# Performance work log

Hardware: AMD Instinct MI355X
Metric: run time of the kernel (lower is better)

## Reference

```python
import jax, jax.numpy as jnp
import numpy as np

B = 1000        # graphs in batch
T_PER = 250     # tasks per graph
M_PER = 50      # machines per graph
N_T = B * T_PER
N_M = B * M_PER
D_T = 16        # INPUT_TASK_DIM
D_M = 8         # INPUT_MACHINE_DIM
H = 128         # hidden_dim
IN_PREV_IDX = 0
TASK_FEAT_IDX = 1
EPS = 1e-5      # BatchNorm eps


def _mk_params(rng):
    def lin(i, o):
        return (rng.standard_normal((i, o)).astype(np.float32) / np.sqrt(i),
                np.zeros(o, np.float32))
    p = {}
    p['bn_t_gamma'] = np.ones(D_T, np.float32); p['bn_t_beta'] = np.zeros(D_T, np.float32)
    p['Wt1'], p['bt1'] = lin(D_T, H); p['Wt2'], p['bt2'] = lin(H, H)
    p['bn_m_gamma'] = np.ones(D_M, np.float32); p['bn_m_beta'] = np.zeros(D_M, np.float32)
    p['Wm1'], p['bm1'] = lin(D_M, H); p['Wm2'], p['bm2'] = lin(H, H)
    p['Wa1'], p['ba1'] = lin(2 * H, H); p['Wa2'], p['ba2'] = lin(H, H)
    p['Wl1'], p['bl1'] = lin(3 * H, H); p['Wl2'], p['bl2'] = lin(H, H)
    p['Wo1'], p['bo1'] = lin(H, H); p['Wo2'], p['bo2'] = lin(H, 1)
    return p


def setup_inputs() -> dict:
    rng = np.random.default_rng(0)
    xt = rng.standard_normal((N_T, D_T)).astype(np.float32)
    # prev-task flag: even task ids are 'prev'
    xt[:, IN_PREV_IDX] = (np.arange(N_T) % 2 == 0).astype(np.float32)
    # per-graph machine assignment in [0, M_PER), or -1 (unassigned) every 10th task
    lm = rng.integers(0, M_PER, N_T)
    lm[np.arange(N_T) % 10 == 0] = -1
    xt[:, TASK_FEAT_IDX] = lm.astype(np.float32)
    xm = rng.standard_normal((N_M, D_M)).astype(np.float32)
    inp = {'x_tasks': jnp.asarray(xt), 'x_machines': jnp.asarray(xm)}
    inp.update({k: jnp.asarray(v) for k, v in _mk_params(rng).items()})
    inp['x_tasks_batch'] = jnp.asarray(np.repeat(np.arange(B), T_PER).astype(np.int32))
    inp['x_machines_batch'] = jnp.asarray(np.repeat(np.arange(B), M_PER).astype(np.int32))
    # labels are tasks 0,5,10,...; prev tasks are even ids -> prev-local index t//2
    # label tasks that are prev: t % 10 == 0 -> prev_tasks_label_idx = 5*arange(N_T//10)
    inp['label_idx'] = jnp.asarray((5 * np.arange(N_T // 10)).astype(np.int32))
    inp['num_graphs'] = B
    return inp


def _bn(x, g, b):
    # BatchNorm1d in training mode: biased batch stats
    mu = x.mean(axis=0)
    var = x.var(axis=0)
    return g * (x - mu) * jax.lax.rsqrt(var + EPS) + b


def _seg_mean(x, seg, n):
    s = jax.ops.segment_sum(x, seg, num_segments=n)
    c = jax.ops.segment_sum(jnp.ones((x.shape[0], 1), x.dtype), seg, num_segments=n)
    return s / jnp.maximum(c, 1.0)


def reference(x_tasks, x_machines, bn_t_gamma, bn_t_beta, Wt1, bt1, Wt2, bt2,
              bn_m_gamma, bn_m_beta, Wm1, bm1, Wm2, bm2,
              Wa1, ba1, Wa2, ba2, Wl1, bl1, Wl2, bl2,
              Wo1, bo1, Wo2, bo2,
              x_tasks_batch, x_machines_batch, label_idx, num_graphs):
    nm = x_machines.shape[0]
    # tasks_select_assignment: local machine id -> global machine row (or pad row nm)
    tm_col = x_tasks[:, TASK_FEAT_IDX]
    cnt_m = jnp.bincount(x_machines_batch, length=num_graphs)
    cum = jnp.cumsum(cnt_m) - cnt_m  # cumulative machines per graph
    task_m = jnp.where(tm_col == -1.0, nm,
                       tm_col.astype(jnp.int32) + cum[x_tasks_batch].astype(jnp.int32))
    # node embeddings: BN -> Linear -> ReLU -> Linear -> ReLU
    th = jax.nn.relu(jax.nn.relu(_bn(x_tasks, bn_t_gamma, bn_t_beta) @ Wt1 + bt1) @ Wt2 + bt2)
    mh = jax.nn.relu(jax.nn.relu(_bn(x_machines, bn_m_gamma, bn_m_beta) @ Wm1 + bm1) @ Wm2 + bm2)
    # global aggregation per graph (scatter_mean) + MLP
    aggr = jnp.concatenate([_seg_mean(th, x_tasks_batch, num_graphs),
                            _seg_mean(mh, x_machines_batch, num_graphs)], axis=1)
    aggr = jax.nn.relu(aggr @ Wa1 + ba1) @ Wa2 + ba2
    # gather machine embedding per task (pad row of zeros for unassigned)
    mh_pad = jnp.concatenate([mh, jnp.zeros((1, H), mh.dtype)], axis=0)
    cat = jnp.concatenate([th, aggr[x_tasks_batch], mh_pad[task_m]], axis=1)  # [N_T, 3H]
    h = jax.nn.relu(cat @ Wl1 + bl1) @ Wl2 + bl2
    out = (jax.nn.relu(h @ Wo1 + bo1) @ Wo2 + bo2)[label_idx]
    return out
```

## Files before the change

kernel.cpp:

```cpp
#include <hip/hip_runtime.h>
#include <hip/hip_bf16.h>

constexpr int B     = 1000;
constexpr int T_PER = 250;
constexpr int M_PER = 50;
constexpr int N_T   = B * T_PER;
constexpr int N_M   = B * M_PER;
constexpr int H     = 128;
constexpr int N_LBL = 25000;
constexpr float EPS = 1e-05f;

constexpr int NB_T = 256;
constexpr int NB_M = 64;
constexpr int NB_P = 64;

constexpr int OFF_PART_T = 0;
constexpr int OFF_PART_M = OFF_PART_T + NB_T * 32;
constexpr int OFF_AT     = OFF_PART_M + NB_M * 16;
constexpr int OFF_BT     = OFF_AT + 16;
constexpr int OFF_AM     = OFF_BT + 16;
constexpr int OFF_BM     = OFF_AM + 8;
constexpr int OFF_BT1F   = OFF_BM + 8;
constexpr int OFF_BM1F   = OFF_BT1F + 128;
constexpr int OFF_MEANT  = OFF_BM1F + 128;
constexpr int OFF_MEANM  = OFF_MEANT + B * H;
constexpr int OFF_HALF   = OFF_MEANM + B * H;
constexpr int HO_WT1  = 0;
constexpr int HO_WT2  = 4096;
constexpr int HO_WM1  = 20480;
constexpr int HO_WM2  = 24576;
constexpr int HO_WA1  = 40960;
constexpr int HO_WA2  = 73728;
constexpr int HO_WL1  = 90112;
constexpr int HO_WL2  = 139264;
constexpr int HO_WO1  = 155648;

typedef _Float16 f16x8 __attribute__((ext_vector_type(8)));
typedef _Float16 f16x4 __attribute__((ext_vector_type(4)));
typedef float f32x4 __attribute__((ext_vector_type(4)));

#define MFMA16(a, b, c) __builtin_amdgcn_mfma_f32_16x16x32_f16(a, b, c, 0, 0, 0)

template <int C, int NB>
__device__ __forceinline__ void stats_body(const float* __restrict__ x, int nelem,
                                           float* __restrict__ part, int blk, int t,
                                           float* ls, float* lq) {
    float s = 0.f, q = 0.f;
    for (int e = blk * 256 + t; e < nelem; e += NB * 256) {
        float v = x[e];
        s += v;
        q += v * v;
    }
    ls[t] = s; lq[t] = q;
    __syncthreads();
    if (t < C) {
        float S = 0.f, Q = 0.f;
        for (int u = t; u < 256; u += C) { S += ls[u]; Q += lq[u]; }
        part[blk * 2 * C + t] = S;
        part[blk * 2 * C + C + t] = Q;
    }
}

__device__ __forceinline__ void cvt_tr(const float* __restrict__ src, _Float16* __restrict__ dst,
                                       int K, int Kp, int tid, int nt) {
    for (int idx = tid; idx < 128 * Kp; idx += nt) {
        int c = idx / Kp, k = idx - c * Kp;
        float v = (k < K) ? src[k * 128 + c] : 0.f;
        dst[idx] = (_Float16)v;
    }
}

__global__ __launch_bounds__(256) void stats_prep_kernel(
        const float* __restrict__ xt, const float* __restrict__ xm,
        const float* __restrict__ Wt1, const float* __restrict__ Wt2,
        const float* __restrict__ Wm1, const float* __restrict__ Wm2,
        const float* __restrict__ Wa1, const float* __restrict__ Wa2,
        const float* __restrict__ Wl1, const float* __restrict__ Wl2,
        const float* __restrict__ Wo1,
        float* __restrict__ wsf, _Float16* __restrict__ wh) {
    __shared__ float ls[256], lq[256];
    const int bid = blockIdx.x, t = threadIdx.x;
    if (bid < NB_T) {
        stats_body<16, NB_T>(xt, N_T * 16, wsf + OFF_PART_T, bid, t, ls, lq);
    } else if (bid < NB_T + NB_M) {
        stats_body<8, NB_M>(xm, N_M * 8, wsf + OFF_PART_M, bid - NB_T, t, ls, lq);
    } else {
        const int tid = (bid - NB_T - NB_M) * 256 + t;
        const int nt = NB_P * 256;
        cvt_tr(Wt1, wh + HO_WT1, 16, 32, tid, nt);
        cvt_tr(Wt2, wh + HO_WT2, 128, 128, tid, nt);
        cvt_tr(Wm1, wh + HO_WM1, 8, 32, tid, nt);
        cvt_tr(Wm2, wh + HO_WM2, 128, 128, tid, nt);
        cvt_tr(Wa1, wh + HO_WA1, 256, 256, tid, nt);
        cvt_tr(Wa2, wh + HO_WA2, 128, 128, tid, nt);
        cvt_tr(Wl1, wh + HO_WL1, 384, 384, tid, nt);
        cvt_tr(Wl2, wh + HO_WL2, 128, 128, tid, nt);
        cvt_tr(Wo1, wh + HO_WO1, 128, 128, tid, nt);
    }
}

__global__ __launch_bounds__(256) void finalize_kernel(
        const float* __restrict__ gt, const float* __restrict__ btb,
        const float* __restrict__ gm, const float* __restrict__ bmb,
        const float* __restrict__ Wt1, const float* __restrict__ bt1,
        const float* __restrict__ Wm1, const float* __restrict__ bm1,
        float* __restrict__ ws) {
    __shared__ float red[256];
    __shared__ float statT[32], statM[16];
    __shared__ float shT[16], shM[8];
    const int t = threadIdx.x;
    {
        const int slot = t & 31, chunk = t >> 5;
        const float* p = ws + OFF_PART_T;
        float s = 0.f;
        for (int b = chunk * 32; b < chunk * 32 + 32; b++) s += p[b * 32 + slot];
        red[t] = s;
    }
    __syncthreads();
    if (t < 32) {
        float v = 0.f;
#pragma unroll
        for (int c = 0; c < 8; c++) v += red[t + 32 * c];
        statT[t] = v;
    }
    __syncthreads();
    {
        float s = 0.f;
        if (t < 128) {
            const int slot = t & 15, chunk = t >> 4;
            const float* p = ws + OFF_PART_M;
            for (int b = chunk * 8; b < chunk * 8 + 8; b++) s += p[b * 16 + slot];
        }
        red[t] = s;
    }
    __syncthreads();
    if (t < 16) {
        float v = 0.f;
#pragma unroll
        for (int c = 0; c < 8; c++) v += red[t + 16 * c];
        statM[t] = v;
    }
    __syncthreads();
    if (t < 16) {
        float mu  = statT[t] / (float)N_T;
        float var = statT[16 + t] / (float)N_T - mu * mu;
        float a   = gt[t] * rsqrtf(var + EPS);
        ws[OFF_AT + t] = a;
        float b = btb[t] - mu * a;
        ws[OFF_BT + t] = b;
        shT[t] = b;
    } else if (t < 24) {
        int c = t - 16;
        float mu  = statM[c] / (float)N_M;
        float var = statM[8 + c] / (float)N_M - mu * mu;
        float a   = gm[c] * rsqrtf(var + EPS);
        ws[OFF_AM + c] = a;
        float b = bmb[c] - mu * a;
        ws[OFF_BM + c] = b;
        shM[c] = b;
    }
    __syncthreads();
    if (t < 128) {
        float s = bt1[t];
#pragma unroll
        for (int k = 0; k < 16; k++) s += shT[k] * Wt1[k * 128 + t];
        ws[OFF_BT1F + t] = s;
    } else {
        int c = t - 128;
        float s = bm1[c];
#pragma unroll
        for (int k = 0; k < 8; k++) s += shM[k] * Wm1[k * 128 + c];
        ws[OFF_BM1F + c] = s;
    }
}

__device__ __forceinline__ void zacc(f32x4 acc[4][2]) {
#pragma unroll
    for (int rg = 0; rg < 4; rg++)
#pragma unroll
        for (int mi = 0; mi < 2; mi++) acc[rg][mi] = (f32x4){0.f, 0.f, 0.f, 0.f};
}

__device__ __forceinline__ void ld32(f16x8 w[2], const _Float16* __restrict__ WT,
                                     int m0, int r, int gq) {
#pragma unroll
    for (int mi = 0; mi < 2; mi++)
        w[mi] = *(const f16x8*)(WT + ((m0 + mi) * 16 + r) * 32 + gq * 8);
}

__device__ __forceinline__ void ld128(f16x8 w[2][4], const _Float16* __restrict__ WT,
                                      int lda, int k0, int m0, int r, int gq) {
#pragma unroll
    for (int mi = 0; mi < 2; mi++)
#pragma unroll
        for (int ks = 0; ks < 4; ks++)
            w[mi][ks] = *(const f16x8*)(WT + ((m0 + mi) * 16 + r) * lda + k0 + ks * 32 + gq * 8);
}

__device__ __forceinline__ void mm32(const f16x8 w[2], const _Float16* __restrict__ act,
                                     int rstride, int r, int gq, f32x4 acc[4][2]) {
#pragma unroll
    for (int rg = 0; rg < 4; rg++) {
        const f16x8 bf = *(const f16x8*)(act + (rg * 16 + r) * rstride + gq * 8);
        acc[rg][0] = MFMA16(w[0], bf, acc[rg][0]);
        acc[rg][1] = MFMA16(w[1], bf, acc[rg][1]);
    }
}

__device__ __forceinline__ void mm128(const f16x8 w[2][4], const _Float16* __restrict__ act,
                                      int rstride, int r, int gq, f32x4 acc[4][2]) {
#pragma unroll
    for (int rg = 0; rg < 4; rg++)
#pragma unroll
        for (int ks = 0; ks < 4; ks++) {
            const f16x8 bf = *(const f16x8*)(act + (rg * 16 + r) * rstride + ks * 32 + gq * 8);
            acc[rg][0] = MFMA16(w[0][ks], bf, acc[rg][0]);
            acc[rg][1] = MFMA16(w[1][ks], bf, acc[rg][1]);
        }
}

__device__ __forceinline__ void epi_cs(const f32x4 acc[4][2], const f32x4 bv[2],
                                       _Float16* __restrict__ dst, int dstride,
                                       int m0, int r, int gq, bool relu) {
#pragma unroll
    for (int rg = 0; rg < 4; rg++)
#pragma unroll
        for (int mi = 0; mi < 2; mi++) {
            f16x4 hv;
#pragma unroll
            for (int j = 0; j < 4; j++) {
                float v = acc[rg][mi][j] + bv[mi][j];
                if (relu) v = fmaxf(v, 0.f);
                hv[j] = (_Float16)v;
            }
            *(f16x4*)(dst + (rg * 16 + r) * dstride + (m0 + mi) * 16 + gq * 4) = hv;
        }
}

template <int CIN, int ROWS, int PASSES>
__device__ __forceinline__ void seg_body(const float* __restrict__ x, const float* __restrict__ scaleA,
        const _Float16* __restrict__ W1T, const float* __restrict__ b1,
        const _Float16* __restrict__ W2T, const float* __restrict__ b2,
        float* __restrict__ meanout, int g, int t,
        _Float16* __restrict__ xs, _Float16* __restrict__ h1s) {
    const int lane = t & 63, wave = t >> 6;
    const int r = lane & 15, gq = lane >> 4;
    const int m0 = 2 * wave;
    f16x8 w1[2], w2[2][4];
    ld32(w1, W1T, m0, r, gq);
    ld128(w2, W2T, 128, 0, m0, r, gq);
    f32x4 b1v[2], b2v[2];
#pragma unroll
    for (int mi = 0; mi < 2; mi++) {
        b1v[mi] = *(const f32x4*)(b1 + (m0 + mi) * 16 + gq * 4);
        b2v[mi] = *(const f32x4*)(b2 + (m0 + mi) * 16 + gq * 4);
    }
    const int jrow = (CIN == 16) ? (t >> 2) : (t >> 1);
    const int part = (CIN == 16) ? (t & 3) : (t & 1);
    const bool stager = (CIN == 16) ? true : (t < 128);
    f32x4 av = {0.f, 0.f, 0.f, 0.f};
    if (stager) av = *(const f32x4*)(scaleA + part * 4);
    f16x4 z4; z4[0] = z4[1] = z4[2] = z4[3] = (_Float16)0.f;
    if (stager) {
        if (CIN == 16) {
            *(f16x4*)(xs + jrow * 40 + 16 + part * 4) = z4;
        } else {
#pragma unroll
            for (int q = 0; q < 3; q++)
                *(f16x4*)(xs + jrow * 40 + 8 + part * 12 + q * 4) = z4;
        }
    }
    float4 xr = {0.f, 0.f, 0.f, 0.f};
    if (stager) {
        int cl = (jrow < ROWS) ? jrow : (ROWS - 1);
        xr = *(const float4*)(x + (g * ROWS + cl) * CIN + part * 4);
    }
    f32x4 rs[2];
    rs[0] = (f32x4){0.f, 0.f, 0.f, 0.f};
    rs[1] = (f32x4){0.f, 0.f, 0.f, 0.f};
    for (int p = 0; p < PASSES; p++) {
        if (stager) {
            const bool valid = (p * 64 + jrow) < ROWS;
            f16x4 hv;
            hv[0] = (_Float16)(valid ? av[0] * xr.x : 0.f);
            hv[1] = (_Float16)(valid ? av[1] * xr.y : 0.f);
            hv[2] = (_Float16)(valid ? av[2] * xr.z : 0.f);
            hv[3] = (_Float16)(valid ? av[3] * xr.w : 0.f);
            *(f16x4*)(xs + jrow * 40 + part * 4) = hv;
        }
        __syncthreads();
        if (p + 1 < PASSES && stager) {
            int lr = (p + 1) * 64 + jrow;
            int cl = (lr < ROWS) ? lr : (ROWS - 1);
            xr = *(const float4*)(x + (g * ROWS + cl) * CIN + part * 4);
        }
        f32x4 acc[4][2];
        zacc(acc);
        mm32(w1, xs, 40, r, gq, acc);
        epi_cs(acc, b1v, h1s, 136, m0, r, gq, true);
        __syncthreads();
        zacc(acc);
        mm128(w2, h1s, 136, r, gq, acc);
#pragma unroll
        for (int rg = 0; rg < 4; rg++) {
            const bool vr = (p * 64 + rg * 16 + r) < ROWS;
#pragma unroll
            for (int mi = 0; mi < 2; mi++)
#pragma unroll
                for (int j = 0; j < 4; j++) {
                    float v = fmaxf(acc[rg][mi][j] + b2v[mi][j], 0.f);
                    rs[mi][j] += vr ? v : 0.f;
                }
        }
    }
#pragma unroll
    for (int mi = 0; mi < 2; mi++)
#pragma unroll
        for (int j = 0; j < 4; j++) {
            float v = rs[mi][j];
            v += __shfl_xor(v, 1); v += __shfl_xor(v, 2);
            v += __shfl_xor(v, 4); v += __shfl_xor(v, 8);
            rs[mi][j] = v;
        }
    if (r == 0) {
        constexpr float inv = 1.f / (float)ROWS;
#pragma unroll
        for (int mi = 0; mi < 2; mi++) {
            f32x4 st = rs[mi] * inv;
            *(f32x4*)(meanout + g * H + (m0 + mi) * 16 + gq * 4) = st;
        }
    }
}

__global__ __launch_bounds__(256) void seg_fused(const float* __restrict__ xt, const float* __restrict__ xm,
        const _Float16* __restrict__ wh, const float* __restrict__ wsf,
        const float* __restrict__ bt2, const float* __restrict__ bm2,
        float* __restrict__ meanT, float* __restrict__ meanM) {
    __shared__ __attribute__((aligned(16))) _Float16 xs[64 * 40];
    __shared__ __attribute__((aligned(16))) _Float16 h1s[64 * 136];
    if (blockIdx.x < B)
        seg_body<16, T_PER, 4>(xt, wsf + OFF_AT, wh + HO_WT1, wsf + OFF_BT1F,
                               wh + HO_WT2, bt2, meanT, blockIdx.x, threadIdx.x, xs, h1s);
    else
        seg_body<8, M_PER, 1>(xm, wsf + OFF_AM, wh + HO_WM1, wsf + OFF_BM1F,
                              wh + HO_WM2, bm2, meanM, blockIdx.x - B, threadIdx.x, xs, h1s);
}

__global__ __launch_bounds__(256) void aggr_kernel(const float* __restrict__ meanT, const float* __restrict__ meanM,
        const _Float16* __restrict__ Wa1T, const float* __restrict__ ba1,
        const _Float16* __restrict__ Wa2T, const float* __restrict__ ba2,
        const _Float16* __restrict__ Wl1T, const float* __restrict__ bl1,
        float* __restrict__ agg2) {
    __shared__ __attribute__((aligned(16))) _Float16 cin[16 * 264];
    __shared__ __attribute__((aligned(16))) _Float16 h1s[16 * 136];
    __shared__ __attribute__((aligned(16))) _Float16 ags[16 * 136];
    const int t = threadIdx.x, lane = t & 63, wave = t >> 6;
    const int r = lane & 15, gq = lane >> 4;
    const int m0 = 2 * wave;
    const int g0 = blockIdx.x * 16;
    f16x8 wa1[2][8], wa2[2][4], wl1b[2][4];
#pragma unroll
    for (int mi = 0; mi < 2; mi++)
#pragma unroll
        for (int ks = 0; ks < 8; ks++)
            wa1[mi][ks] = *(const f16x8*)(Wa1T + ((m0 + mi) * 16 + r) * 256 + ks * 32 + gq * 8);
    ld128(wa2, Wa2T, 128, 0, m0, r, gq);
    ld128(wl1b, Wl1T, 384, 128, m0, r, gq);
    f32x4 b1v[2], b2v[2], blv[2];
#pragma unroll
    for (int mi = 0; mi < 2; mi++) {
        b1v[mi] = *(const f32x4*)(ba1 + (m0 + mi) * 16 + gq * 4);
        b2v[mi] = *(const f32x4*)(ba2 + (m0 + mi) * 16 + gq * 4);
        blv[mi] = *(const f32x4*)(bl1 + (m0 + mi) * 16 + gq * 4);
    }
    for (int e = t; e < 16 * 64; e += 256) {
        int j = e >> 6, c4 = e & 63;
        int g = g0 + j;
        float4 v = {0.f, 0.f, 0.f, 0.f};
        if (g < B) v = (c4 < 32) ? *(const float4*)(meanT + g * H + c4 * 4)
                                 : *(const float4*)(meanM + g * H + (c4 - 32) * 4);
        f16x4 hv;
        hv[0] = (_Float16)v.x; hv[1] = (_Float16)v.y; hv[2] = (_Float16)v.z; hv[3] = (_Float16)v.w;
        *(f16x4*)(cin + j * 264 + c4 * 4) = hv;
    }
    __syncthreads();
    f32x4 a0 = {0.f, 0.f, 0.f, 0.f}, a1 = {0.f, 0.f, 0.f, 0.f};
    {
        const _Float16* bp = cin + r * 264 + gq * 8;
#pragma unroll
        for (int ks = 0; ks < 8; ks++) {
            const f16x8 bf = *(const f16x8*)(bp + ks * 32);
            a0 = MFMA16(wa1[0][ks], bf, a0);
            a1 = MFMA16(wa1[1][ks], bf, a1);
        }
    }
    {
        f16x4 h0, h1v;
#pragma unroll
        for (int j = 0; j < 4; j++) {
            h0[j]  = (_Float16)fmaxf(a0[j] + b1v[0][j], 0.f);
            h1v[j] = (_Float16)fmaxf(a1[j] + b1v[1][j], 0.f);
        }
        *(f16x4*)(h1s + r * 136 + m0 * 16 + gq * 4) = h0;
        *(f16x4*)(h1s + r * 136 + (m0 + 1) * 16 + gq * 4) = h1v;
    }
    __syncthreads();
    a0 = (f32x4){0.f, 0.f, 0.f, 0.f}; a1 = (f32x4){0.f, 0.f, 0.f, 0.f};
    {
        const _Float16* bp = h1s + r * 136 + gq * 8;
#pragma unroll
        for (int ks = 0; ks < 4; ks++) {
            const f16x8 bf = *(const f16x8*)(bp + ks * 32);
            a0 = MFMA16(wa2[0][ks], bf, a0);
            a1 = MFMA16(wa2[1][ks], bf, a1);
        }
    }
    {
        f16x4 h0, h1v;
#pragma unroll
        for (int j = 0; j < 4; j++) {
            h0[j]  = (_Float16)(a0[j] + b2v[0][j]);
            h1v[j] = (_Float16)(a1[j] + b2v[1][j]);
        }
        *(f16x4*)(ags + r * 136 + m0 * 16 + gq * 4) = h0;
        *(f16x4*)(ags + r * 136 + (m0 + 1) * 16 + gq * 4) = h1v;
    }
    __syncthreads();
    a0 = (f32x4){0.f, 0.f, 0.f, 0.f}; a1 = (f32x4){0.f, 0.f, 0.f, 0.f};
    {
        const _Float16* bp = ags + r * 136 + gq * 8;
#pragma unroll
        for (int ks = 0; ks < 4; ks++) {
            const f16x8 bf = *(const f16x8*)(bp + ks * 32);
            a0 = MFMA16(wl1b[0][ks], bf, a0);
            a1 = MFMA16(wl1b[1][ks], bf, a1);
        }
    }
    if (g0 + r < B) {
        *(f32x4*)(agg2 + (g0 + r) * H + m0 * 16 + gq * 4) = a0 + blv[0];
        *(f32x4*)(agg2 + (g0 + r) * H + (m0 + 1) * 16 + gq * 4) = a1 + blv[1];
    }
}

__global__ __launch_bounds__(256) void label_kernel(
        const float* __restrict__ xt, const float* __restrict__ xm,
        const float* __restrict__ scT, const float* __restrict__ scM,
        const _Float16* __restrict__ Wt1T, const float* __restrict__ bt1f,
        const _Float16* __restrict__ Wt2T, const float* __restrict__ bt2,
        const _Float16* __restrict__ Wm1T, const float* __restrict__ bm1f,
        const _Float16* __restrict__ Wm2T, const float* __restrict__ bm2,
        const _Float16* __restrict__ Wl1T,
        const _Float16* __restrict__ Wl2T, const float* __restrict__ bl2,
        const _Float16* __restrict__ Wo1T, const float* __restrict__ bo1,
        const float* __restrict__ Wo2, const float* __restrict__ bo2,
        const float* __restrict__ agg2,
        const int* __restrict__ tbatch, const int* __restrict__ lidx,
        float* __restrict__ out) {
    __shared__ __attribute__((aligned(16))) _Float16 xs_t[64 * 40];
    __shared__ __attribute__((aligned(16))) _Float16 xs_m[64 * 40];
    __shared__ __attribute__((aligned(16))) _Float16 h1s[64 * 136];
    __shared__ __attribute__((aligned(16))) _Float16 cat[64 * 264];
    __shared__ float psum[4][64];
    __shared__ int ridx[64], gidx[64], midx[64];
    const int t = threadIdx.x;
    const int lane = t & 63, wave = t >> 6;
    const int r = lane & 15, gq = lane >> 4;
    const int m0 = 2 * wave;
    if (t < 64) {
        int i = blockIdx.x * 64 + t;
        int rr = (i < N_LBL) ? lidx[i] : 0;
        ridx[t] = rr;
        int gg = tbatch[rr];
        gidx[t] = gg;
        float tv = xt[rr * 16 + 1];
        midx[t] = (tv == -1.0f) ? -1 : ((int)tv + gg * M_PER);
    }
    __syncthreads();
    f16x4 z4; z4[0] = z4[1] = z4[2] = z4[3] = (_Float16)0.f;
    {
        int j = t >> 2, part = t & 3;
        f32x4 avt = *(const f32x4*)(scT + part * 4);
        float4 v = *(const float4*)(xt + ridx[j] * 16 + part * 4);
        f16x4 hv;
        hv[0] = (_Float16)(avt[0] * v.x); hv[1] = (_Float16)(avt[1] * v.y);
        hv[2] = (_Float16)(avt[2] * v.z); hv[3] = (_Float16)(avt[3] * v.w);
        *(f16x4*)(xs_t + j * 40 + part * 4) = hv;
        *(f16x4*)(xs_t + j * 40 + 16 + part * 4) = z4;
    }
    if (t < 128) {
        int j = t >> 1, part = t & 1;
        f32x4 avm = *(const f32x4*)(scM + part * 4);
        int m = midx[j];
        f16x4 hv = z4;
        if (m >= 0) {
            float4 v = *(const float4*)(xm + m * 8 + part * 4);
            hv[0] = (_Float16)(avm[0] * v.x); hv[1] = (_Float16)(avm[1] * v.y);
            hv[2] = (_Float16)(avm[2] * v.z); hv[3] = (_Float16)(avm[3] * v.w);
        }
        *(f16x4*)(xs_m + j * 40 + part * 4) = hv;
#pragma unroll
        for (int q = 0; q < 3; q++)
            *(f16x4*)(xs_m + j * 40 + 8 + part * 12 + q * 4) = z4;
    }
    __syncthreads();
    f32x4 agg2v[4][2];
#pragma unroll
    for (int rg = 0; rg < 4; rg++)
#pragma unroll
        for (int mi = 0; mi < 2; mi++)
            agg2v[rg][mi] = *(const f32x4*)(agg2 + gidx[rg * 16 + r] * H + (m0 + mi) * 16 + gq * 4);
    f32x4 acc[4][2];
    f16x8 wt1[2]; ld32(wt1, Wt1T, m0, r, gq);
    f16x8 wt2[2][4]; ld128(wt2, Wt2T, 128, 0, m0, r, gq);
    f32x4 bva[2], bvb[2];
#pragma unroll
    for (int mi = 0; mi < 2; mi++) {
        bva[mi] = *(const f32x4*)(bt1f + (m0 + mi) * 16 + gq * 4);
        bvb[mi] = *(const f32x4*)(bt2 + (m0 + mi) * 16 + gq * 4);
    }
    zacc(acc);
    mm32(wt1, xs_t, 40, r, gq, acc);
    epi_cs(acc, bva, h1s, 136, m0, r, gq, true);
    f16x8 wm1[2]; ld32(wm1, Wm1T, m0, r, gq);
    __syncthreads();
    zacc(acc);
    mm128(wt2, h1s, 136, r, gq, acc);
    epi_cs(acc, bvb, cat, 264, m0, r, gq, true);
    f16x8 wm2[2][4]; ld128(wm2, Wm2T, 128, 0, m0, r, gq);
    __syncthreads();
#pragma unroll
    for (int mi = 0; mi < 2; mi++) {
        bva[mi] = *(const f32x4*)(bm1f + (m0 + mi) * 16 + gq * 4);
        bvb[mi] = *(const f32x4*)(bm2 + (m0 + mi) * 16 + gq * 4);
    }
    zacc(acc);
    mm32(wm1, xs_m, 40, r, gq, acc);
    epi_cs(acc, bva, h1s, 136, m0, r, gq, true);
    f16x8 wl1a[2][4]; ld128(wl1a, Wl1T, 384, 0, m0, r, gq);
    __syncthreads();
    zacc(acc);
    mm128(wm2, h1s, 136, r, gq, acc);
#pragma unroll
    for (int rg = 0; rg < 4; rg++) {
        const bool sent = (midx[rg * 16 + r] < 0);
#pragma unroll
        for (int mi = 0; mi < 2; mi++) {
            f16x4 hv;
#pragma unroll
            for (int j = 0; j < 4; j++) {
                float v = fmaxf(acc[rg][mi][j] + bvb[mi][j], 0.f);
                hv[j] = (_Float16)(sent ? 0.f : v);
            }
            *(f16x4*)(cat + (rg * 16 + r) * 264 + 128 + (m0 + mi) * 16 + gq * 4) = hv;
        }
    }
    f16x8 wl1c[2][4]; ld128(wl1c, Wl1T, 384, 256, m0, r, gq);
    __syncthreads();
    zacc(acc);
    mm128(wl1a, cat, 264, r, gq, acc);
    mm128(wl1c, cat + 128, 264, r, gq, acc);
#pragma unroll
    for (int rg = 0; rg < 4; rg++)
#pragma unroll
        for (int mi = 0; mi < 2; mi++) {
            f16x4 hv;
#pragma unroll
            for (int j = 0; j < 4; j++)
                hv[j] = (_Float16)fmaxf(acc[rg][mi][j] + agg2v[rg][mi][j], 0.f);
            *(f16x4*)(h1s + (rg * 16 + r) * 136 + (m0 + mi) * 16 + gq * 4) = hv;
        }
    f16x8 wl2[2][4]; ld128(wl2, Wl2T, 128, 0, m0, r, gq);
    __syncthreads();
#pragma unroll
    for (int mi = 0; mi < 2; mi++) bva[mi] = *(const f32x4*)(bl2 + (m0 + mi) * 16 + gq * 4);
    zacc(acc);
    mm128(wl2, h1s, 136, r, gq, acc);
    epi_cs(acc, bva, cat, 264, m0, r, gq, false);
    f16x8 wo1[2][4]; ld128(wo1, Wo1T, 128, 0, m0, r, gq);
    __syncthreads();
#pragma unroll
    for (int mi = 0; mi < 2; mi++) bva[mi] = *(const f32x4*)(bo1 + (m0 + mi) * 16 + gq * 4);
    f32x4 wo2v[2];
#pragma unroll
    for (int mi = 0; mi < 2; mi++) wo2v[mi] = *(const f32x4*)(Wo2 + (m0 + mi) * 16 + gq * 4);
    zacc(acc);
    mm128(wo1, cat, 264, r, gq, acc);
#pragma unroll
    for (int rg = 0; rg < 4; rg++) {
        float pv = 0.f;
#pragma unroll
        for (int mi = 0; mi < 2; mi++)
#pragma unroll
            for (int j = 0; j < 4; j++)
                pv += fmaxf(acc[rg][mi][j] + bva[mi][j], 0.f) * wo2v[mi][j];
        pv += __shfl_xor(pv, 16);
        pv += __shfl_xor(pv, 32);
        if (lane < 16) psum[wave][rg * 16 + lane] = pv;
    }
    __syncthreads();
    if (t < 64) {
        int i = blockIdx.x * 64 + t;
        if (i < N_LBL)
            out[i] = psum[0][t] + psum[1][t] + psum[2][t] + psum[3][t] + bo2[0];
    }
}

extern "C" void kernel_launch(void* const* d_in, const int* in_sizes, int n_in,
                              void* d_out, int out_size, void* d_ws, size_t ws_size,
                              hipStream_t stream) {
    const float* xt  = (const float*)d_in[0];
    const float* xm  = (const float*)d_in[1];
    const float* gt  = (const float*)d_in[2];
    const float* btb = (const float*)d_in[3];
    const float* Wt1 = (const float*)d_in[4];  const float* bt1 = (const float*)d_in[5];
    const float* Wt2 = (const float*)d_in[6];  const float* bt2 = (const float*)d_in[7];
    const float* gm  = (const float*)d_in[8];  const float* bmb = (const float*)d_in[9];
    const float* Wm1 = (const float*)d_in[10]; const float* bm1 = (const float*)d_in[11];
    const float* Wm2 = (const float*)d_in[12]; const float* bm2 = (const float*)d_in[13];
    const float* Wa1 = (const float*)d_in[14]; const float* ba1 = (const float*)d_in[15];
    const float* Wa2 = (const float*)d_in[16]; const float* ba2 = (const float*)d_in[17];
    const float* Wl1 = (const float*)d_in[18]; const float* bl1 = (const float*)d_in[19];
    const float* Wl2 = (const float*)d_in[20]; const float* bl2 = (const float*)d_in[21];
    const float* Wo1 = (const float*)d_in[22]; const float* bo1 = (const float*)d_in[23];
    const float* Wo2 = (const float*)d_in[24]; const float* bo2 = (const float*)d_in[25];
    const int* tb  = (const int*)d_in[26];
    const int* lix = (const int*)d_in[28];
    float* wsf = (float*)d_ws;
    _Float16* wh = (_Float16*)(wsf + OFF_HALF);
    float* outp = (float*)d_out;

    stats_prep_kernel<<<NB_T + NB_M + NB_P, 256, 0, stream>>>(
        xt, xm, Wt1, Wt2, Wm1, Wm2, Wa1, Wa2, Wl1, Wl2, Wo1, wsf, wh);
    finalize_kernel<<<1, 256, 0, stream>>>(gt, btb, gm, bmb, Wt1, bt1, Wm1, bm1, wsf);
    seg_fused<<<2 * B, 256, 0, stream>>>(xt, xm, wh, wsf, bt2, bm2,
                                         wsf + OFF_MEANT, wsf + OFF_MEANM);
    aggr_kernel<<<(B + 15) / 16, 256, 0, stream>>>(wsf + OFF_MEANT, wsf + OFF_MEANM,
                                                   wh + HO_WA1, ba1, wh + HO_WA2, ba2,
                                                   wh + HO_WL1, bl1, wsf + OFF_MEANT);
    label_kernel<<<(N_LBL + 63) / 64, 256, 0, stream>>>(xt, xm,
                                                        wsf + OFF_AT, wsf + OFF_AM,
                                                        wh + HO_WT1, wsf + OFF_BT1F, wh + HO_WT2, bt2,
                                                        wh + HO_WM1, wsf + OFF_BM1F, wh + HO_WM2, bm2,
                                                        wh + HO_WL1,
                                                        wh + HO_WL2, bl2,
                                                        wh + HO_WO1, bo1, Wo2, bo2,
                                                        wsf + OFF_MEANT, tb, lix, outp);
}
```

Measured before the change: 74.12 us.

## Split task segment-mean across four blocks per graph with fp16 pre-converted inputs

```diff
diff --git a/kernel.cpp b/kernel.cpp
--- a/kernel.cpp
+++ b/kernel.cpp
@@ -1,5 +1,4 @@
 #include <hip/hip_runtime.h>
-#include <hip/hip_bf16.h>
 
 constexpr int B     = 1000;
 constexpr int T_PER = 250;
@@ -34,6 +33,8 @@
 constexpr int HO_WL1  = 90112;
 constexpr int HO_WL2  = 139264;
 constexpr int HO_WO1  = 155648;
+constexpr int HO_XT16 = 172032;
+constexpr int HO_XM16 = HO_XT16 + N_T * 16;
 
 typedef _Float16 f16x8 __attribute__((ext_vector_type(8)));
 typedef _Float16 f16x4 __attribute__((ext_vector_type(4)));
@@ -42,7 +43,8 @@
 #define MFMA16(a, b, c) __builtin_amdgcn_mfma_f32_16x16x32_f16(a, b, c, 0, 0, 0)
 
 template <int C, int NB>
-__device__ __forceinline__ void stats_body(const float* __restrict__ x, int nelem,
+__device__ __forceinline__ void stats_body(const float* __restrict__ x,
+                                           _Float16* __restrict__ x16, int nelem,
                                            float* __restrict__ part, int blk, int t,
                                            float* ls, float* lq) {
     float s = 0.f, q = 0.f;
@@ -50,6 +52,7 @@
         float v = x[e];
         s += v;
         q += v * v;
+        x16[e] = (_Float16)v;
     }
     ls[t] = s; lq[t] = q;
     __syncthreads();
@@ -72,6 +75,7 @@
 
 __global__ __launch_bounds__(256) void stats_prep_kernel(
         const float* __restrict__ xt, const float* __restrict__ xm,
+        _Float16* __restrict__ xt16, _Float16* __restrict__ xm16,
         const float* __restrict__ Wt1, const float* __restrict__ Wt2,
         const float* __restrict__ Wm1, const float* __restrict__ Wm2,
         const float* __restrict__ Wa1, const float* __restrict__ Wa2,
@@ -81,12 +85,14 @@
     __shared__ float ls[256], lq[256];
     const int bid = blockIdx.x, t = threadIdx.x;
     if (bid < NB_T) {
-        stats_body<16, NB_T>(xt, N_T * 16, wsf + OFF_PART_T, bid, t, ls, lq);
+        stats_body<16, NB_T>(xt, xt16, N_T * 16, wsf + OFF_PART_T, bid, t, ls, lq);
     } else if (bid < NB_T + NB_M) {
-        stats_body<8, NB_M>(xm, N_M * 8, wsf + OFF_PART_M, bid - NB_T, t, ls, lq);
+        stats_body<8, NB_M>(xm, xm16, N_M * 8, wsf + OFF_PART_M, bid - NB_T, t, ls, lq);
     } else {
         const int tid = (bid - NB_T - NB_M) * 256 + t;
         const int nt = NB_P * 256;
+        float* mz = wsf + OFF_MEANT;
+        for (int i = tid; i < B * H; i += nt) mz[i] = 0.f;
         cvt_tr(Wt1, wh + HO_WT1, 16, 32, tid, nt);
         cvt_tr(Wt2, wh + HO_WT2, 128, 128, tid, nt);
         cvt_tr(Wm1, wh + HO_WM1, 8, 32, tid, nt);
@@ -197,13 +203,11 @@
             w[mi][ks] = *(const f16x8*)(WT + ((m0 + mi) * 16 + r) * lda + k0 + ks * 32 + gq * 8);
 }
 
-__device__ __forceinline__ void mm32(const f16x8 w[2], const _Float16* __restrict__ act,
-                                     int rstride, int r, int gq, f32x4 acc[4][2]) {
+__device__ __forceinline__ void mm32g(const f16x8 w[2], const f16x8 xb[4], f32x4 acc[4][2]) {
 #pragma unroll
     for (int rg = 0; rg < 4; rg++) {
-        const f16x8 bf = *(const f16x8*)(act + (rg * 16 + r) * rstride + gq * 8);
-        acc[rg][0] = MFMA16(w[0], bf, acc[rg][0]);
-        acc[rg][1] = MFMA16(w[1], bf, acc[rg][1]);
+        acc[rg][0] = MFMA16(w[0], xb[rg], acc[rg][0]);
+        acc[rg][1] = MFMA16(w[1], xb[rg], acc[rg][1]);
     }
 }
 
@@ -237,80 +241,73 @@
         }
 }
 
-template <int CIN, int ROWS, int PASSES>
-__device__ __forceinline__ void seg_body(const float* __restrict__ x, const float* __restrict__ scaleA,
-        const _Float16* __restrict__ W1T, const float* __restrict__ b1,
+template <int CIN, int ROWS, bool ATOMIC>
+__device__ __forceinline__ void seg_body(
+        const _Float16* __restrict__ x16, const float* __restrict__ sa,
+        const _Float16* __restrict__ W1T, const float* __restrict__ b1f,
         const _Float16* __restrict__ W2T, const float* __restrict__ b2,
-        float* __restrict__ meanout, int g, int t,
-        _Float16* __restrict__ xs, _Float16* __restrict__ h1s) {
+        float* __restrict__ outp, int g, int r0, int t,
+        _Float16* __restrict__ h1s) {
     const int lane = t & 63, wave = t >> 6;
     const int r = lane & 15, gq = lane >> 4;
     const int m0 = 2 * wave;
-    f16x8 w1[2], w2[2][4];
-    ld32(w1, W1T, m0, r, gq);
-    ld128(w2, W2T, 128, 0, m0, r, gq);
+    f16x8 z8;
+#pragma unroll
+    for (int e = 0; e < 8; e++) z8[e] = (_Float16)0.f;
+    f16x8 w1[2]; ld32(w1, W1T, m0, r, gq);
+    f16x8 w2[2][4]; ld128(w2, W2T, 128, 0, m0, r, gq);
+    if (gq * 8 < CIN) {
+        f32x4 s0 = *(const f32x4*)(sa + gq * 8);
+        f32x4 s1 = *(const f32x4*)(sa + gq * 8 + 4);
+#pragma unroll
+        for (int mi = 0; mi < 2; mi++)
+#pragma unroll
+            for (int e = 0; e < 4; e++) {
+                w1[mi][e]     = (_Float16)((float)w1[mi][e] * s0[e]);
+                w1[mi][4 + e] = (_Float16)((float)w1[mi][4 + e] * s1[e]);
+            }
+    }
+    f16x8 xb[4];
+#pragma unroll
+    for (int rg = 0; rg < 4; rg++) {
+        int row = r0 + rg * 16 + r;
+        int cl = (row < ROWS) ? row : (ROWS - 1);
+        if (CIN == 16) xb[rg] = (gq < 2) ? *(const f16x8*)(x16 + (g * ROWS + cl) * 16 + gq * 8) : z8;
+        else           xb[rg] = (gq == 0) ? *(const f16x8*)(x16 + (g * ROWS + cl) * 8) : z8;
+    }
     f32x4 b1v[2], b2v[2];
 #pragma unroll
     for (int mi = 0; mi < 2; mi++) {
-        b1v[mi] = *(const f32x4*)(b1 + (m0 + mi) * 16 + gq * 4);
+        b1v[mi] = *(const f32x4*)(b1f + (m0 + mi) * 16 + gq * 4);
         b2v[mi] = *(const f32x4*)(b2 + (m0 + mi) * 16 + gq * 4);
     }
-    const int jrow = (CIN == 16) ? (t >> 2) : (t >> 1);
-    const int part = (CIN == 16) ? (t & 3) : (t & 1);
-    const bool stager = (CIN == 16) ? true : (t < 128);
-    f32x4 av = {0.f, 0.f, 0.f, 0.f};
-    if (stager) av = *(const f32x4*)(scaleA + part * 4);
-    f16x4 z4; z4[0] = z4[1] = z4[2] = z4[3] = (_Float16)0.f;
-    if (stager) {
-        if (CIN == 16) {
-            *(f16x4*)(xs + jrow * 40 + 16 + part * 4) = z4;
-        } else {
-#pragma unroll
-            for (int q = 0; q < 3; q++)
-                *(f16x4*)(xs + jrow * 40 + 8 + part * 12 + q * 4) = z4;
-        }
-    }
-    float4 xr = {0.f, 0.f, 0.f, 0.f};
-    if (stager) {
-        int cl = (jrow < ROWS) ? jrow : (ROWS - 1);
-        xr = *(const float4*)(x + (g * ROWS + cl) * CIN + part * 4);
-    }
+    f32x4 acc[4][2];
+    zacc(acc);
+    mm32g(w1, xb, acc);
+    epi_cs(acc, b1v, h1s, 136, m0, r, gq, true);
+    __syncthreads();
+    zacc(acc);
+    mm128(w2, h1s, 136, r, gq, acc);
     f32x4 rs[2];
     rs[0] = (f32x4){0.f, 0.f, 0.f, 0.f};
     rs[1] = (f32x4){0.f, 0.f, 0.f, 0.f};
-    for (int p = 0; p < PASSES; p++) {
-        if (stager) {
-            const bool valid = (p * 64 + jrow) < ROWS;
-            f16x4 hv;
-            hv[0] = (_Float16)(valid ? av[0] * xr.x : 0.f);
-            hv[1] = (_Float16)(valid ? av[1] * xr.y : 0.f);
-            hv[2] = (_Float16)(valid ? av[2] * xr.z : 0.f);
-            hv[3] = (_Float16)(valid ? av[3] * xr.w : 0.f);
-            *(f16x4*)(xs + jrow * 40 + part * 4) = hv;
-        }
-        __syncthreads();
-        if (p + 1 < PASSES && stager) {
-            int lr = (p + 1) * 64 + jrow;
-            int cl = (lr < ROWS) ? lr : (ROWS - 1);
-            xr = *(const float4*)(x + (g * ROWS + cl) * CIN + part * 4);
-        }
-        f32x4 acc[4][2];
-        zacc(acc);
-        mm32(w1, xs, 40, r, gq, acc);
-        epi_cs(acc, b1v, h1s, 136, m0, r, gq, true);
-        __syncthreads();
-        zacc(acc);
-        mm128(w2, h1s, 136, r, gq, acc);
+    if (r0 + 64 <= ROWS) {
+#pragma unroll
+        for (int rg = 0; rg < 4; rg++)
+#pragma unroll
+            for (int mi = 0; mi < 2; mi++)
+#pragma unroll
+                for (int j = 0; j < 4; j++)
+                    rs[mi][j] += fmaxf(acc[rg][mi][j] + b2v[mi][j], 0.f);
+    } else {
 #pragma unroll
         for (int rg = 0; rg < 4; rg++) {
-            const bool vr = (p * 64 + rg * 16 + r) < ROWS;
+            const float mk = ((r0 + rg * 16 + r) < ROWS) ? 1.f : 0.f;
 #pragma unroll
             for (int mi = 0; mi < 2; mi++)
 #pragma unroll
-                for (int j = 0; j < 4; j++) {
-                    float v = fmaxf(acc[rg][mi][j] + b2v[mi][j], 0.f);
-                    rs[mi][j] += vr ? v : 0.f;
-                }
+                for (int j = 0; j < 4; j++)
+                    rs[mi][j] = fmaf(fmaxf(acc[rg][mi][j] + b2v[mi][j], 0.f), mk, rs[mi][j]);
         }
     }
 #pragma unroll
@@ -324,26 +321,37 @@
         }
     if (r == 0) {
         constexpr float inv = 1.f / (float)ROWS;
-#pragma unroll
-        for (int mi = 0; mi < 2; mi++) {
-            f32x4 st = rs[mi] * inv;
-            *(f32x4*)(meanout + g * H + (m0 + mi) * 16 + gq * 4) = st;
-        }
-    }
-}
-
-__global__ __launch_bounds__(256) void seg_fused(const float* __restrict__ xt, const float* __restrict__ xm,
+        if (ATOMIC) {
+#pragma unroll
+            for (int mi = 0; mi < 2; mi++)
+#pragma unroll
+                for (int j = 0; j < 4; j++)
+                    atomicAdd(outp + g * H + (m0 + mi) * 16 + gq * 4 + j, rs[mi][j] * inv);
+        } else {
+#pragma unroll
+            for (int mi = 0; mi < 2; mi++) {
+                f32x4 st = rs[mi] * inv;
+                *(f32x4*)(outp + g * H + (m0 + mi) * 16 + gq * 4) = st;
+            }
+        }
+    }
+}
+
+__global__ __launch_bounds__(256) void seg_fused(
+        const _Float16* __restrict__ xt16, const _Float16* __restrict__ xm16,
         const _Float16* __restrict__ wh, const float* __restrict__ wsf,
         const float* __restrict__ bt2, const float* __restrict__ bm2,
         float* __restrict__ meanT, float* __restrict__ meanM) {
-    __shared__ __attribute__((aligned(16))) _Float16 xs[64 * 40];
     __shared__ __attribute__((aligned(16))) _Float16 h1s[64 * 136];
-    if (blockIdx.x < B)
-        seg_body<16, T_PER, 4>(xt, wsf + OFF_AT, wh + HO_WT1, wsf + OFF_BT1F,
-                               wh + HO_WT2, bt2, meanT, blockIdx.x, threadIdx.x, xs, h1s);
+    const int bid = blockIdx.x;
+    if (bid < 4 * B)
+        seg_body<16, T_PER, true>(xt16, wsf + OFF_AT, wh + HO_WT1, wsf + OFF_BT1F,
+                                  wh + HO_WT2, bt2, meanT, bid >> 2, (bid & 3) * 64,
+                                  threadIdx.x, h1s);
     else
-        seg_body<8, M_PER, 1>(xm, wsf + OFF_AM, wh + HO_WM1, wsf + OFF_BM1F,
-                              wh + HO_WM2, bm2, meanM, blockIdx.x - B, threadIdx.x, xs, h1s);
+        seg_body<8, M_PER, false>(xm16, wsf + OFF_AM, wh + HO_WM1, wsf + OFF_BM1F,
+                                  wh + HO_WM2, bm2, meanM, bid - 4 * B, 0,
+                                  threadIdx.x, h1s);
 }
 
 __global__ __launch_bounds__(256) void aggr_kernel(const float* __restrict__ meanT, const float* __restrict__ meanM,
@@ -443,7 +451,8 @@
 }
 
 __global__ __launch_bounds__(256) void label_kernel(
-        const float* __restrict__ xt, const float* __restrict__ xm,
+        const float* __restrict__ xt,
+        const _Float16* __restrict__ xt16, const _Float16* __restrict__ xm16,
         const float* __restrict__ scT, const float* __restrict__ scM,
         const _Float16* __restrict__ Wt1T, const float* __restrict__ bt1f,
         const _Float16* __restrict__ Wt2T, const float* __restrict__ bt2,
@@ -456,8 +465,6 @@
         const float* __restrict__ agg2,
         const int* __restrict__ tbatch, const int* __restrict__ lidx,
         float* __restrict__ out) {
-    __shared__ __attribute__((aligned(16))) _Float16 xs_t[64 * 40];
-    __shared__ __attribute__((aligned(16))) _Float16 xs_m[64 * 40];
     __shared__ __attribute__((aligned(16))) _Float16 h1s[64 * 136];
     __shared__ __attribute__((aligned(16))) _Float16 cat[64 * 264];
     __shared__ float psum[4][64];
@@ -476,33 +483,17 @@
         midx[t] = (tv == -1.0f) ? -1 : ((int)tv + gg * M_PER);
     }
     __syncthreads();
-    f16x4 z4; z4[0] = z4[1] = z4[2] = z4[3] = (_Float16)0.f;
-    {
-        int j = t >> 2, part = t & 3;
-        f32x4 avt = *(const f32x4*)(scT + part * 4);
-        float4 v = *(const float4*)(xt + ridx[j] * 16 + part * 4);
-        f16x4 hv;
-        hv[0] = (_Float16)(avt[0] * v.x); hv[1] = (_Float16)(avt[1] * v.y);
-        hv[2] = (_Float16)(avt[2] * v.z); hv[3] = (_Float16)(avt[3] * v.w);
-        *(f16x4*)(xs_t + j * 40 + part * 4) = hv;
-        *(f16x4*)(xs_t + j * 40 + 16 + part * 4) = z4;
-    }
-    if (t < 128) {
-        int j = t >> 1, part = t & 1;
-        f32x4 avm = *(const f32x4*)(scM + part * 4);
-        int m = midx[j];
-        f16x4 hv = z4;
-        if (m >= 0) {
-            float4 v = *(const float4*)(xm + m * 8 + part * 4);
-            hv[0] = (_Float16)(avm[0] * v.x); hv[1] = (_Float16)(avm[1] * v.y);
-            hv[2] = (_Float16)(avm[2] * v.z); hv[3] = (_Float16)(avm[3] * v.w);
-        }
-        *(f16x4*)(xs_m + j * 40 + part * 4) = hv;
-#pragma unroll
-        for (int q = 0; q < 3; q++)
-            *(f16x4*)(xs_m + j * 40 + 8 + part * 12 + q * 4) = z4;
-    }
-    __syncthreads();
+    f16x8 z8;
+#pragma unroll
+    for (int e = 0; e < 8; e++) z8[e] = (_Float16)0.f;
+    f16x8 xbT[4], xbM[4];
+#pragma unroll
+    for (int rg = 0; rg < 4; rg++) {
+        int rr = ridx[rg * 16 + r];
+        xbT[rg] = (gq < 2) ? *(const f16x8*)(xt16 + rr * 16 + gq * 8) : z8;
+        int mm = midx[rg * 16 + r];
+        xbM[rg] = (gq == 0 && mm >= 0) ? *(const f16x8*)(xm16 + mm * 8) : z8;
+    }
     f32x4 agg2v[4][2];
 #pragma unroll
     for (int rg = 0; rg < 4; rg++)
@@ -511,6 +502,17 @@
             agg2v[rg][mi] = *(const f32x4*)(agg2 + gidx[rg * 16 + r] * H + (m0 + mi) * 16 + gq * 4);
     f32x4 acc[4][2];
     f16x8 wt1[2]; ld32(wt1, Wt1T, m0, r, gq);
+    if (gq < 2) {
+        f32x4 s0 = *(const f32x4*)(scT + gq * 8);
+        f32x4 s1 = *(const f32x4*)(scT + gq * 8 + 4);
+#pragma unroll
+        for (int mi = 0; mi < 2; mi++)
+#pragma unroll
+            for (int e = 0; e < 4; e++) {
+                wt1[mi][e]     = (_Float16)((float)wt1[mi][e] * s0[e]);
+                wt1[mi][4 + e] = (_Float16)((float)wt1[mi][4 + e] * s1[e]);
+            }
+    }
     f16x8 wt2[2][4]; ld128(wt2, Wt2T, 128, 0, m0, r, gq);
     f32x4 bva[2], bvb[2];
 #pragma unroll
@@ -519,9 +521,20 @@
         bvb[mi] = *(const f32x4*)(bt2 + (m0 + mi) * 16 + gq * 4);
     }
     zacc(acc);
-    mm32(wt1, xs_t, 40, r, gq, acc);
+    mm32g(wt1, xbT, acc);
     epi_cs(acc, bva, h1s, 136, m0, r, gq, true);
     f16x8 wm1[2]; ld32(wm1, Wm1T, m0, r, gq);
+    if (gq == 0) {
+        f32x4 s0 = *(const f32x4*)(scM);
+        f32x4 s1 = *(const f32x4*)(scM + 4);
+#pragma unroll
+        for (int mi = 0; mi < 2; mi++)
+#pragma unroll
+            for (int e = 0; e < 4; e++) {
+                wm1[mi][e]     = (_Float16)((float)wm1[mi][e] * s0[e]);
+                wm1[mi][4 + e] = (_Float16)((float)wm1[mi][4 + e] * s1[e]);
+            }
+    }
     __syncthreads();
     zacc(acc);
     mm128(wt2, h1s, 136, r, gq, acc);
@@ -534,7 +547,7 @@
         bvb[mi] = *(const f32x4*)(bm2 + (m0 + mi) * 16 + gq * 4);
     }
     zacc(acc);
-    mm32(wm1, xs_m, 40, r, gq, acc);
+    mm32g(wm1, xbM, acc);
     epi_cs(acc, bva, h1s, 136, m0, r, gq, true);
     f16x8 wl1a[2][4]; ld128(wl1a, Wl1T, 384, 0, m0, r, gq);
     __syncthreads();
@@ -627,17 +640,19 @@
     const int* lix = (const int*)d_in[28];
     float* wsf = (float*)d_ws;
     _Float16* wh = (_Float16*)(wsf + OFF_HALF);
+    _Float16* xt16 = wh + HO_XT16;
+    _Float16* xm16 = wh + HO_XM16;
     float* outp = (float*)d_out;
 
     stats_prep_kernel<<<NB_T + NB_M + NB_P, 256, 0, stream>>>(
-        xt, xm, Wt1, Wt2, Wm1, Wm2, Wa1, Wa2, Wl1, Wl2, Wo1, wsf, wh);
+        xt, xm, xt16, xm16, Wt1, Wt2, Wm1, Wm2, Wa1, Wa2, Wl1, Wl2, Wo1, wsf, wh);
     finalize_kernel<<<1, 256, 0, stream>>>(gt, btb, gm, bmb, Wt1, bt1, Wm1, bm1, wsf);
-    seg_fused<<<2 * B, 256, 0, stream>>>(xt, xm, wh, wsf, bt2, bm2,
+    seg_fused<<<5 * B, 256, 0, stream>>>(xt16, xm16, wh, wsf, bt2, bm2,
                                          wsf + OFF_MEANT, wsf + OFF_MEANM);
     aggr_kernel<<<(B + 15) / 16, 256, 0, stream>>>(wsf + OFF_MEANT, wsf + OFF_MEANM,
                                                    wh + HO_WA1, ba1, wh + HO_WA2, ba2,
                                                    wh + HO_WL1, bl1, wsf + OFF_MEANT);
-    label_kernel<<<(N_LBL + 63) / 64, 256, 0, stream>>>(xt, xm,
+    label_kernel<<<(N_LBL + 63) / 64, 256, 0, stream>>>(xt, xt16, xm16,
                                                         wsf + OFF_AT, wsf + OFF_AM,
                                                         wh + HO_WT1, wsf + OFF_BT1F, wh + HO_WT2, bt2,
                                                         wh + HO_WM1, wsf + OFF_BM1F, wh + HO_WM2, bm2,
```

After: 90.44 us. 1.22x slower.
